# Performance work log

Hardware: AMD Instinct MI355X
Metric: run time of the kernel (lower is better)

## Reference

```python
import jax, jax.numpy as jnp
import numpy as np

THRESH = 0.1
BN_EPS = 1e-5
B, N, C_IN, C_HID, C_OUT = 4096, 128, 64, 256, 128


def setup_inputs() -> dict:
    key = jax.random.key(0)
    ks = jax.random.split(key, 10)
    a = jax.random.uniform(ks[0], (B, N, N), dtype=jnp.float32)
    v = jax.random.normal(ks[1], (B, N, C_IN), dtype=jnp.float32)
    # MLP params: Linear(C_IN->C_HID) + BN + ReLU + Linear(C_HID->C_OUT) + BN + ReLU
    W1 = jax.random.normal(ks[2], (C_IN, C_HID), dtype=jnp.float32) / np.sqrt(C_IN)
    b1 = jnp.zeros((C_HID,), jnp.float32)
    g1 = 1.0 + 0.1 * jax.random.normal(ks[3], (C_HID,), dtype=jnp.float32)
    be1 = 0.1 * jax.random.normal(ks[4], (C_HID,), dtype=jnp.float32)
    rm1 = 0.1 * jax.random.normal(ks[5], (C_HID,), dtype=jnp.float32)
    rv1 = jnp.ones((C_HID,), jnp.float32)
    W2 = jax.random.normal(ks[6], (C_HID, C_OUT), dtype=jnp.float32) / np.sqrt(C_HID)
    b2 = jnp.zeros((C_OUT,), jnp.float32)
    g2 = 1.0 + 0.1 * jax.random.normal(ks[7], (C_OUT,), dtype=jnp.float32)
    be2 = 0.1 * jax.random.normal(ks[8], (C_OUT,), dtype=jnp.float32)
    rm2 = 0.1 * jax.random.normal(ks[9], (C_OUT,), dtype=jnp.float32)
    rv2 = jnp.ones((C_OUT,), jnp.float32)
    return {"a": a, "v": v, "W1": W1, "b1": b1, "g1": g1, "be1": be1, "rm1": rm1, "rv1": rv1,
            "W2": W2, "b2": b2, "g2": g2, "be2": be2, "rm2": rm2, "rv2": rv2}


def reference(a, v, W1, b1, g1, be1, rm1, rv1, W2, b2, g2, be2, rm2, rv2):
    # threshold adjacency
    a_th = (a >= THRESH).astype(v.dtype)            # [B, N, N]
    # D^-0.5 A D^-0.5 as row/col rescaling (equivalent to diag_embed + bmm)
    d_inv_sqrt = jnp.sum(a_th, axis=-1) ** -0.5     # [B, N]
    a_bar = d_inv_sqrt[:, :, None] * a_th * d_inv_sqrt[:, None, :]
    # propagate
    h = jnp.einsum('bnm,bmc->bnc', a_bar, v)        # [B, N, C_IN]
    x = h.reshape(-1, h.shape[-1])                  # [(B N), C_IN]
    # MLP with BatchNorm in eval mode (running stats), dropout is identity in eval
    x = x @ W1 + b1
    x = (x - rm1) * jax.lax.rsqrt(rv1 + BN_EPS) * g1 + be1
    x = jax.nn.relu(x)
    x = x @ W2 + b2
    x = (x - rm2) * jax.lax.rsqrt(rv2 + BN_EPS) * g2 + be2
    x = jax.nn.relu(x)
    return x
```

## Files before the change

kernel.cpp:

```cpp
#include <hip/hip_runtime.h>


#define THRESH 0.1f
#define BN_EPS 1e-5f

typedef __attribute__((ext_vector_type(8))) short bf16x8;
typedef __attribute__((ext_vector_type(4))) float f32x4;

__device__ __forceinline__ unsigned short f2bf(float f) {
    union { float f; unsigned u; } x; x.f = f;
    unsigned r = x.u + 0x7FFFu + ((x.u >> 16) & 1u);
    return (unsigned short)(r >> 16);
}

__device__ __forceinline__ unsigned cvt_pk(float lo, float hi) {
    unsigned r;
    asm("v_cvt_pk_bf16_f32 %0, %1, %2" : "=v"(r) : "v"(lo), "v"(hi));
    return r;
}

__global__ void gcn_prep(const float* __restrict__ W1, const float* __restrict__ b1,
                         const float* __restrict__ g1, const float* __restrict__ be1,
                         const float* __restrict__ rm1, const float* __restrict__ rv1,
                         const float* __restrict__ W2, const float* __restrict__ b2,
                         const float* __restrict__ g2, const float* __restrict__ be2,
                         const float* __restrict__ rm2, const float* __restrict__ rv2,
                         unsigned short* __restrict__ W1s, unsigned short* __restrict__ W2s,
                         float* __restrict__ sh1, float* __restrict__ sh2) {
    int t = blockIdx.x * blockDim.x + threadIdx.x;
    if (t < 256 * 64) {
        int n = t >> 6, kp = t & 63;
        int sp = kp >> 3, lo = kp & 7;
        int s  = sp ^ (n & 7);
        int k2 = s * 8 + lo;
        int r = k2 & 3, aa = (k2 >> 2) & 1, gg = (k2 >> 3) & 3, T = k2 >> 5;
        int k = T * 32 + aa * 16 + gg * 4 + r;
        float sc = g1[n] * rsqrtf(rv1[n] + BN_EPS);
        W1s[t] = f2bf(W1[k * 256 + n] * sc);
    }
    {
        int n = t >> 8, kp = t & 255;
        int sp = kp >> 3, lo = kp & 7;
        int s  = sp ^ (n & 7);
        int k2 = s * 8 + lo;
        int r = k2 & 3, aa = (k2 >> 2) & 1, gg = (k2 >> 3) & 3, T = k2 >> 5;
        int k = T * 32 + aa * 16 + gg * 4 + r;
        float sc = g2[n] * rsqrtf(rv2[n] + BN_EPS);
        W2s[t] = f2bf(W2[k * 128 + n] * sc);
    }
    if (t < 256) {
        float s = g1[t] * rsqrtf(rv1[t] + BN_EPS);
        sh1[t] = (b1[t] - rm1[t]) * s + be1[t];
    }
    if (t < 128) {
        float s = g2[t] * rsqrtf(rv2[t] + BN_EPS);
        sh2[t] = (b2[t] - rm2[t]) * s + be2[t];
    }
}

__global__ void __launch_bounds__(256, 4)
gcn_prop(const float* __restrict__ A, const float* __restrict__ V,
         unsigned short* __restrict__ hP) {
    __shared__ unsigned short s_vtt[64 * 136];

    const int t    = threadIdx.x;
    const int lane = t & 63;
    const int w    = t >> 6;
    const int r16  = lane & 15;
    const int g    = lane >> 4;
    const int b    = blockIdx.x;

    const int mloc  = lane & 31;
    const int chalf = (lane >> 5) * 32;
    const float* vb = V + (size_t)b * 8192 + (size_t)(32 * w + mloc) * 64 + chalf;
    f32x4 pv[8];
#pragma unroll
    for (int q = 0; q < 8; ++q) pv[q] = *(const f32x4*)(vb + 4 * q);

    const float* ab = A + (size_t)b * 16384 + (size_t)(32 * w + r16) * 128;
    bf16x8 afrag[2][4];
    int cnt0 = 0, cnt1 = 0;
#pragma unroll
    for (int mt = 0; mt < 2; ++mt)
#pragma unroll
        for (int ks = 0; ks < 4; ++ks) {
            const float* p = ab + mt * 2048 + ks * 32 + 8 * g;
            f32x4 x0 = *(const f32x4*)p;
            f32x4 x1 = *(const f32x4*)(p + 4);
            union { unsigned short s[8]; bf16x8 v; } u;
            u.s[0] = (x0.x >= THRESH) ? (unsigned short)0x3F80u : (unsigned short)0u;
            u.s[1] = (x0.y >= THRESH) ? (unsigned short)0x3F80u : (unsigned short)0u;
            u.s[2] = (x0.z >= THRESH) ? (unsigned short)0x3F80u : (unsigned short)0u;
            u.s[3] = (x0.w >= THRESH) ? (unsigned short)0x3F80u : (unsigned short)0u;
            u.s[4] = (x1.x >= THRESH) ? (unsigned short)0x3F80u : (unsigned short)0u;
            u.s[5] = (x1.y >= THRESH) ? (unsigned short)0x3F80u : (unsigned short)0u;
            u.s[6] = (x1.z >= THRESH) ? (unsigned short)0x3F80u : (unsigned short)0u;
            u.s[7] = (x1.w >= THRESH) ? (unsigned short)0x3F80u : (unsigned short)0u;
            afrag[mt][ks] = u.v;
            int c = (x0.x >= THRESH) + (x0.y >= THRESH) + (x0.z >= THRESH) + (x0.w >= THRESH)
                  + (x1.x >= THRESH) + (x1.y >= THRESH) + (x1.z >= THRESH) + (x1.w >= THRESH);
            if (mt == 0) cnt0 += c; else cnt1 += c;
        }
    cnt0 += __shfl_xor(cnt0, 16); cnt0 += __shfl_xor(cnt0, 32);
    cnt1 += __shfl_xor(cnt1, 16); cnt1 += __shfl_xor(cnt1, 32);
    const float dinv0 = rsqrtf((float)cnt0);
    const float dinv1 = rsqrtf((float)cnt1);

    {
        float dm = (lane & 16) ? dinv1 : dinv0;
        int m = 32 * w + mloc;
#pragma unroll
        for (int q = 0; q < 8; ++q) {
            int c = chalf + 4 * q;
            s_vtt[(c + 0) * 136 + m] = f2bf(pv[q].x * dm);
            s_vtt[(c + 1) * 136 + m] = f2bf(pv[q].y * dm);
            s_vtt[(c + 2) * 136 + m] = f2bf(pv[q].z * dm);
            s_vtt[(c + 3) * 136 + m] = f2bf(pv[q].w * dm);
        }
    }
    __syncthreads();

    f32x4 acc1[4][2];
#pragma unroll
    for (int ct = 0; ct < 4; ++ct)
#pragma unroll
        for (int mt = 0; mt < 2; ++mt) acc1[ct][mt] = f32x4{0.f, 0.f, 0.f, 0.f};
#pragma unroll
    for (int ks = 0; ks < 4; ++ks)
#pragma unroll
        for (int ct = 0; ct < 4; ++ct) {
            bf16x8 av = *(const bf16x8*)(s_vtt + (ct * 16 + r16) * 136 + ks * 32 + 8 * g);
            acc1[ct][0] = __builtin_amdgcn_mfma_f32_16x16x32_bf16(av, afrag[0][ks], acc1[ct][0], 0, 0, 0);
            acc1[ct][1] = __builtin_amdgcn_mfma_f32_16x16x32_bf16(av, afrag[1][ks], acc1[ct][1], 0, 0, 0);
        }

#pragma unroll
    for (int mt = 0; mt < 2; ++mt) {
        float d = (mt == 0) ? dinv0 : dinv1;
        size_t m = (size_t)(b * 128 + 32 * w + 16 * mt + r16);
#pragma unroll
        for (int ks2 = 0; ks2 < 2; ++ks2) {
            union { unsigned u[4]; bf16x8 v; } pk;
            pk.u[0] = cvt_pk(acc1[2 * ks2][mt][0] * d,     acc1[2 * ks2][mt][1] * d);
            pk.u[1] = cvt_pk(acc1[2 * ks2][mt][2] * d,     acc1[2 * ks2][mt][3] * d);
            pk.u[2] = cvt_pk(acc1[2 * ks2 + 1][mt][0] * d, acc1[2 * ks2 + 1][mt][1] * d);
            pk.u[3] = cvt_pk(acc1[2 * ks2 + 1][mt][2] * d, acc1[2 * ks2 + 1][mt][3] * d);
            *(bf16x8*)(hP + m * 64 + ks2 * 32 + 8 * g) = pk.v;
        }
    }
}

__global__ void __launch_bounds__(512, 2)
gcn_mlp(const unsigned short* __restrict__ hP,
        const unsigned short* __restrict__ W1s, const unsigned short* __restrict__ W2s,
        const float* __restrict__ sh1g, const float* __restrict__ sh2g,
        float* __restrict__ out) {
    __shared__ char smem[99840];
    unsigned short* W1L = (unsigned short*)smem;
    unsigned short* W2L = (unsigned short*)(smem + 32768);
    float* s_sh1 = (float*)(smem + 98304);
    float* s_sh2 = (float*)(smem + 99328);

    const int t    = threadIdx.x;
    const int lane = t & 63;
    const int w    = t >> 6;
    const int r16  = lane & 15;
    const int g    = lane >> 4;

#pragma unroll
    for (int q = 0; q < 4; ++q)
        *(f32x4*)(smem + t * 64 + q * 16) = *(const f32x4*)((const char*)W1s + t * 64 + q * 16);
#pragma unroll
    for (int q = 0; q < 8; ++q)
        *(f32x4*)(smem + 32768 + t * 128 + q * 16) =
            *(const f32x4*)((const char*)W2s + t * 128 + q * 16);
    if (t < 256) s_sh1[t] = sh1g[t];
    if (t < 128) s_sh2[t] = sh2g[t];
    __syncthreads();

    const size_t row00 = (size_t)blockIdx.x * 1024;

#pragma unroll 1
    for (int i = 0; i < 4; ++i) {
        const size_t mb = row00 + (size_t)i * 256 + 32 * w;

        bf16x8 bh[2][2];
#pragma unroll
        for (int mt = 0; mt < 2; ++mt)
#pragma unroll
            for (int ks2 = 0; ks2 < 2; ++ks2)
                bh[mt][ks2] = *(const bf16x8*)(hP + (mb + 16 * mt + r16) * 64 + ks2 * 32 + 8 * g);

        f32x4 acc3[2][8];
#pragma unroll
        for (int mt = 0; mt < 2; ++mt)
#pragma unroll
            for (int ct = 0; ct < 8; ++ct) acc3[mt][ct] = f32x4{0.f, 0.f, 0.f, 0.f};

#pragma unroll
        for (int T = 0; T < 8; ++T) {
            f32x4 a2[2][2];
#pragma unroll
            for (int mt = 0; mt < 2; ++mt)
#pragma unroll
                for (int ctp = 0; ctp < 2; ++ctp) a2[mt][ctp] = f32x4{0.f, 0.f, 0.f, 0.f};
#pragma unroll
            for (int ctp = 0; ctp < 2; ++ctp) {
                int n = (2 * T + ctp) * 16 + r16;
#pragma unroll
                for (int ks2 = 0; ks2 < 2; ++ks2) {
                    int sp = (ks2 * 4 + g) ^ (n & 7);
                    bf16x8 aw = *(const bf16x8*)(W1L + n * 64 + sp * 8);
                    a2[0][ctp] = __builtin_amdgcn_mfma_f32_16x16x32_bf16(aw, bh[0][ks2], a2[0][ctp], 0, 0, 0);
                    a2[1][ctp] = __builtin_amdgcn_mfma_f32_16x16x32_bf16(aw, bh[1][ks2], a2[1][ctp], 0, 0, 0);
                }
            }
            union { unsigned u[4]; bf16x8 v; } af[2];
#pragma unroll
            for (int ctp = 0; ctp < 2; ++ctp) {
                f32x4 sh = *(const f32x4*)(s_sh1 + (2 * T + ctp) * 16 + 4 * g);
#pragma unroll
                for (int mt = 0; mt < 2; ++mt) {
                    float y0 = fmaxf(a2[mt][ctp][0] + sh.x, 0.f);
                    float y1 = fmaxf(a2[mt][ctp][1] + sh.y, 0.f);
                    float y2 = fmaxf(a2[mt][ctp][2] + sh.z, 0.f);
                    float y3 = fmaxf(a2[mt][ctp][3] + sh.w, 0.f);
                    af[mt].u[2 * ctp + 0] = cvt_pk(y0, y1);
                    af[mt].u[2 * ctp + 1] = cvt_pk(y2, y3);
                }
            }
#pragma unroll
            for (int ct3 = 0; ct3 < 8; ++ct3) {
                int n  = ct3 * 16 + r16;
                int sp = (T * 4 + g) ^ (n & 7);
                bf16x8 bw = *(const bf16x8*)(W2L + n * 256 + sp * 8);
                acc3[0][ct3] = __builtin_amdgcn_mfma_f32_16x16x32_bf16(af[0].v, bw, acc3[0][ct3], 0, 0, 0);
                acc3[1][ct3] = __builtin_amdgcn_mfma_f32_16x16x32_bf16(af[1].v, bw, acc3[1][ct3], 0, 0, 0);
            }
        }

        float* ob = out + mb * 128;
#pragma unroll
        for (int ct3 = 0; ct3 < 8; ++ct3) {
            int c = ct3 * 16 + r16;
            float sh = s_sh2[c];
#pragma unroll
            for (int mt = 0; mt < 2; ++mt)
#pragma unroll
                for (int r = 0; r < 4; ++r) {
                    int row = 16 * mt + 4 * g + r;
                    ob[row * 128 + c] = fmaxf(acc3[mt][ct3][r] + sh, 0.f);
                }
        }
    }
}

extern "C" void kernel_launch(void* const* d_in, const int* in_sizes, int n_in,
                              void* d_out, int out_size, void* d_ws, size_t ws_size,
                              hipStream_t stream) {
    (void)in_sizes; (void)n_in; (void)out_size; (void)ws_size;
    const float* a   = (const float*)d_in[0];
    const float* v   = (const float*)d_in[1];
    const float* W1  = (const float*)d_in[2];
    const float* b1  = (const float*)d_in[3];
    const float* g1  = (const float*)d_in[4];
    const float* be1 = (const float*)d_in[5];
    const float* rm1 = (const float*)d_in[6];
    const float* rv1 = (const float*)d_in[7];
    const float* W2  = (const float*)d_in[8];
    const float* b2  = (const float*)d_in[9];
    const float* g2  = (const float*)d_in[10];
    const float* be2 = (const float*)d_in[11];
    const float* rm2 = (const float*)d_in[12];
    const float* rv2 = (const float*)d_in[13];

    char* ws = (char*)d_ws;
    unsigned short* W1s = (unsigned short*)ws;
    unsigned short* W2s = (unsigned short*)(ws + 32768);
    float* sh1 = (float*)(ws + 98304);
    float* sh2 = (float*)(ws + 99328);
    unsigned short* hP = (unsigned short*)(ws + 102400);

    gcn_prep<<<128, 256, 0, stream>>>(W1, b1, g1, be1, rm1, rv1,
                                      W2, b2, g2, be2, rm2, rv2,
                                      W1s, W2s, sh1, sh2);
    gcn_prop<<<4096, 256, 0, stream>>>(a, v, hP);
    gcn_mlp<<<512, 512, 0, stream>>>(hP, W1s, W2s, sh1, sh2, (float*)d_out);
}
```

Measured before the change: 202.7 us.

## Fuse graph propagation and MLP into one persistent kernel

Merges the propagation kernel and the MLP kernel into a single kernel. Each 512-thread block handles 16 graphs, two at a time, and feeds the bf16 propagated features straight from registers into the MLP. This removes the global write and re-read of the intermediate hidden buffer and one kernel launch. In exchange, occupancy drops to one large block per CU and the loads for the next graph happen serially after the output stores, which may expose memory latency.

```diff
diff --git a/kernel.cpp b/kernel.cpp
--- a/kernel.cpp
+++ b/kernel.cpp
@@ -58,114 +58,26 @@
     }
 }
 
-__global__ void __launch_bounds__(256, 4)
-gcn_prop(const float* __restrict__ A, const float* __restrict__ V,
-         unsigned short* __restrict__ hP) {
-    __shared__ unsigned short s_vtt[64 * 136];
+__global__ void __launch_bounds__(512, 1)
+gcn_fused(const float* __restrict__ A, const float* __restrict__ V,
+          const unsigned short* __restrict__ W1s, const unsigned short* __restrict__ W2s,
+          const float* __restrict__ sh1g, const float* __restrict__ sh2g,
+          float* __restrict__ out) {
+    __shared__ char smem[134656];
+    unsigned short* W1L = (unsigned short*)smem;
+    unsigned short* W2L = (unsigned short*)(smem + 32768);
+    float* s_sh1 = (float*)(smem + 133120);
+    float* s_sh2 = (float*)(smem + 134144);
 
     const int t    = threadIdx.x;
     const int lane = t & 63;
     const int w    = t >> 6;
     const int r16  = lane & 15;
     const int g    = lane >> 4;
-    const int b    = blockIdx.x;
-
-    const int mloc  = lane & 31;
-    const int chalf = (lane >> 5) * 32;
-    const float* vb = V + (size_t)b * 8192 + (size_t)(32 * w + mloc) * 64 + chalf;
-    f32x4 pv[8];
-#pragma unroll
-    for (int q = 0; q < 8; ++q) pv[q] = *(const f32x4*)(vb + 4 * q);
-
-    const float* ab = A + (size_t)b * 16384 + (size_t)(32 * w + r16) * 128;
-    bf16x8 afrag[2][4];
-    int cnt0 = 0, cnt1 = 0;
-#pragma unroll
-    for (int mt = 0; mt < 2; ++mt)
-#pragma unroll
-        for (int ks = 0; ks < 4; ++ks) {
-            const float* p = ab + mt * 2048 + ks * 32 + 8 * g;
-            f32x4 x0 = *(const f32x4*)p;
-            f32x4 x1 = *(const f32x4*)(p + 4);
-            union { unsigned short s[8]; bf16x8 v; } u;
-            u.s[0] = (x0.x >= THRESH) ? (unsigned short)0x3F80u : (unsigned short)0u;
-            u.s[1] = (x0.y >= THRESH) ? (unsigned short)0x3F80u : (unsigned short)0u;
-            u.s[2] = (x0.z >= THRESH) ? (unsigned short)0x3F80u : (unsigned short)0u;
-            u.s[3] = (x0.w >= THRESH) ? (unsigned short)0x3F80u : (unsigned short)0u;
-            u.s[4] = (x1.x >= THRESH) ? (unsigned short)0x3F80u : (unsigned short)0u;
-            u.s[5] = (x1.y >= THRESH) ? (unsigned short)0x3F80u : (unsigned short)0u;
-            u.s[6] = (x1.z >= THRESH) ? (unsigned short)0x3F80u : (unsigned short)0u;
-            u.s[7] = (x1.w >= THRESH) ? (unsigned short)0x3F80u : (unsigned short)0u;
-            afrag[mt][ks] = u.v;
-            int c = (x0.x >= THRESH) + (x0.y >= THRESH) + (x0.z >= THRESH) + (x0.w >= THRESH)
-                  + (x1.x >= THRESH) + (x1.y >= THRESH) + (x1.z >= THRESH) + (x1.w >= THRESH);
-            if (mt == 0) cnt0 += c; else cnt1 += c;
-        }
-    cnt0 += __shfl_xor(cnt0, 16); cnt0 += __shfl_xor(cnt0, 32);
-    cnt1 += __shfl_xor(cnt1, 16); cnt1 += __shfl_xor(cnt1, 32);
-    const float dinv0 = rsqrtf((float)cnt0);
-    const float dinv1 = rsqrtf((float)cnt1);
-
-    {
-        float dm = (lane & 16) ? dinv1 : dinv0;
-        int m = 32 * w + mloc;
-#pragma unroll
-        for (int q = 0; q < 8; ++q) {
-            int c = chalf + 4 * q;
-            s_vtt[(c + 0) * 136 + m] = f2bf(pv[q].x * dm);
-            s_vtt[(c + 1) * 136 + m] = f2bf(pv[q].y * dm);
-            s_vtt[(c + 2) * 136 + m] = f2bf(pv[q].z * dm);
-            s_vtt[(c + 3) * 136 + m] = f2bf(pv[q].w * dm);
-        }
-    }
-    __syncthreads();
-
-    f32x4 acc1[4][2];
-#pragma unroll
-    for (int ct = 0; ct < 4; ++ct)
-#pragma unroll
-        for (int mt = 0; mt < 2; ++mt) acc1[ct][mt] = f32x4{0.f, 0.f, 0.f, 0.f};
-#pragma unroll
-    for (int ks = 0; ks < 4; ++ks)
-#pragma unroll
-        for (int ct = 0; ct < 4; ++ct) {
-            bf16x8 av = *(const bf16x8*)(s_vtt + (ct * 16 + r16) * 136 + ks * 32 + 8 * g);
-            acc1[ct][0] = __builtin_amdgcn_mfma_f32_16x16x32_bf16(av, afrag[0][ks], acc1[ct][0], 0, 0, 0);
-            acc1[ct][1] = __builtin_amdgcn_mfma_f32_16x16x32_bf16(av, afrag[1][ks], acc1[ct][1], 0, 0, 0);
-        }
-
-#pragma unroll
-    for (int mt = 0; mt < 2; ++mt) {
-        float d = (mt == 0) ? dinv0 : dinv1;
-        size_t m = (size_t)(b * 128 + 32 * w + 16 * mt + r16);
-#pragma unroll
-        for (int ks2 = 0; ks2 < 2; ++ks2) {
-            union { unsigned u[4]; bf16x8 v; } pk;
-            pk.u[0] = cvt_pk(acc1[2 * ks2][mt][0] * d,     acc1[2 * ks2][mt][1] * d);
-            pk.u[1] = cvt_pk(acc1[2 * ks2][mt][2] * d,     acc1[2 * ks2][mt][3] * d);
-            pk.u[2] = cvt_pk(acc1[2 * ks2 + 1][mt][0] * d, acc1[2 * ks2 + 1][mt][1] * d);
-            pk.u[3] = cvt_pk(acc1[2 * ks2 + 1][mt][2] * d, acc1[2 * ks2 + 1][mt][3] * d);
-            *(bf16x8*)(hP + m * 64 + ks2 * 32 + 8 * g) = pk.v;
-        }
-    }
-}
-
-__global__ void __launch_bounds__(512, 2)
-gcn_mlp(const unsigned short* __restrict__ hP,
-        const unsigned short* __restrict__ W1s, const unsigned short* __restrict__ W2s,
-        const float* __restrict__ sh1g, const float* __restrict__ sh2g,
-        float* __restrict__ out) {
-    __shared__ char smem[99840];
-    unsigned short* W1L = (unsigned short*)smem;
-    unsigned short* W2L = (unsigned short*)(smem + 32768);
-    float* s_sh1 = (float*)(smem + 98304);
-    float* s_sh2 = (float*)(smem + 99328);
-
-    const int t    = threadIdx.x;
-    const int lane = t & 63;
-    const int w    = t >> 6;
-    const int r16  = lane & 15;
-    const int g    = lane >> 4;
+    const int bs   = w >> 2;
+    const int wl   = w & 3;
+
+    unsigned short* vt = (unsigned short*)(smem + 98304) + bs * (64 * 136);
 
 #pragma unroll
     for (int q = 0; q < 4; ++q)
@@ -176,20 +88,95 @@
             *(const f32x4*)((const char*)W2s + t * 128 + q * 16);
     if (t < 256) s_sh1[t] = sh1g[t];
     if (t < 128) s_sh2[t] = sh2g[t];
+
+    const size_t b00 = (size_t)blockIdx.x * 16;
+
+    const int mloc  = lane & 31;
+    const int chalf = (lane >> 5) * 32;
+
+    bf16x8 afrag[2][4];
+    float dinv0, dinv1;
+    {
+        const size_t b = b00 + bs;
+        const float* vb = V + b * 8192 + (size_t)(32 * wl + mloc) * 64 + chalf;
+        f32x4 pv[8];
+#pragma unroll
+        for (int q = 0; q < 8; ++q) pv[q] = *(const f32x4*)(vb + 4 * q);
+
+        const float* ab = A + b * 16384 + (size_t)(32 * wl + r16) * 128;
+        int cnt0 = 0, cnt1 = 0;
+#pragma unroll
+        for (int mt = 0; mt < 2; ++mt)
+#pragma unroll
+            for (int ks = 0; ks < 4; ++ks) {
+                const float* p = ab + mt * 2048 + ks * 32 + 8 * g;
+                f32x4 x0 = *(const f32x4*)p;
+                f32x4 x1 = *(const f32x4*)(p + 4);
+                union { unsigned short s[8]; bf16x8 v; } u;
+                u.s[0] = (x0.x >= THRESH) ? (unsigned short)0x3F80u : (unsigned short)0u;
+                u.s[1] = (x0.y >= THRESH) ? (unsigned short)0x3F80u : (unsigned short)0u;
+                u.s[2] = (x0.z >= THRESH) ? (unsigned short)0x3F80u : (unsigned short)0u;
+                u.s[3] = (x0.w >= THRESH) ? (unsigned short)0x3F80u : (unsigned short)0u;
+                u.s[4] = (x1.x >= THRESH) ? (unsigned short)0x3F80u : (unsigned short)0u;
+                u.s[5] = (x1.y >= THRESH) ? (unsigned short)0x3F80u : (unsigned short)0u;
+                u.s[6] = (x1.z >= THRESH) ? (unsigned short)0x3F80u : (unsigned short)0u;
+                u.s[7] = (x1.w >= THRESH) ? (unsigned short)0x3F80u : (unsigned short)0u;
+                afrag[mt][ks] = u.v;
+                int c = (x0.x >= THRESH) + (x0.y >= THRESH) + (x0.z >= THRESH) + (x0.w >= THRESH)
+                      + (x1.x >= THRESH) + (x1.y >= THRESH) + (x1.z >= THRESH) + (x1.w >= THRESH);
+                if (mt == 0) cnt0 += c; else cnt1 += c;
+            }
+        cnt0 += __shfl_xor(cnt0, 16); cnt0 += __shfl_xor(cnt0, 32);
+        cnt1 += __shfl_xor(cnt1, 16); cnt1 += __shfl_xor(cnt1, 32);
+        dinv0 = rsqrtf((float)cnt0);
+        dinv1 = rsqrtf((float)cnt1);
+
+        float dm = (lane & 16) ? dinv1 : dinv0;
+        int m = 32 * wl + mloc;
+#pragma unroll
+        for (int q = 0; q < 8; ++q) {
+            int c = chalf + 4 * q;
+            vt[(c + 0) * 136 + m] = f2bf(pv[q].x * dm);
+            vt[(c + 1) * 136 + m] = f2bf(pv[q].y * dm);
+            vt[(c + 2) * 136 + m] = f2bf(pv[q].z * dm);
+            vt[(c + 3) * 136 + m] = f2bf(pv[q].w * dm);
+        }
+    }
     __syncthreads();
 
-    const size_t row00 = (size_t)blockIdx.x * 1024;
-
 #pragma unroll 1
-    for (int i = 0; i < 4; ++i) {
-        const size_t mb = row00 + (size_t)i * 256 + 32 * w;
-
+    for (int it = 0; it < 8; ++it) {
+        const size_t b  = b00 + it * 2 + bs;
+        const size_t mb = (size_t)(32 * wl);
+
+        f32x4 acc1[4][2];
+#pragma unroll
+        for (int ct = 0; ct < 4; ++ct)
+#pragma unroll
+            for (int mt = 0; mt < 2; ++mt) acc1[ct][mt] = f32x4{0.f, 0.f, 0.f, 0.f};
+#pragma unroll
+        for (int ks = 0; ks < 4; ++ks)
+#pragma unroll
+            for (int ct = 0; ct < 4; ++ct) {
+                bf16x8 av = *(const bf16x8*)(vt + (ct * 16 + r16) * 136 + ks * 32 + 8 * g);
+                acc1[ct][0] = __builtin_amdgcn_mfma_f32_16x16x32_bf16(av, afrag[0][ks], acc1[ct][0], 0, 0, 0);
+                acc1[ct][1] = __builtin_amdgcn_mfma_f32_16x16x32_bf16(av, afrag[1][ks], acc1[ct][1], 0, 0, 0);
+            }
         bf16x8 bh[2][2];
 #pragma unroll
-        for (int mt = 0; mt < 2; ++mt)
-#pragma unroll
-            for (int ks2 = 0; ks2 < 2; ++ks2)
-                bh[mt][ks2] = *(const bf16x8*)(hP + (mb + 16 * mt + r16) * 64 + ks2 * 32 + 8 * g);
+        for (int mt = 0; mt < 2; ++mt) {
+            float d = (mt == 0) ? dinv0 : dinv1;
+#pragma unroll
+            for (int ks2 = 0; ks2 < 2; ++ks2) {
+                union { unsigned u[4]; bf16x8 v; } pk;
+                pk.u[0] = cvt_pk(acc1[2 * ks2][mt][0] * d,     acc1[2 * ks2][mt][1] * d);
+                pk.u[1] = cvt_pk(acc1[2 * ks2][mt][2] * d,     acc1[2 * ks2][mt][3] * d);
+                pk.u[2] = cvt_pk(acc1[2 * ks2 + 1][mt][0] * d, acc1[2 * ks2 + 1][mt][1] * d);
+                pk.u[3] = cvt_pk(acc1[2 * ks2 + 1][mt][2] * d, acc1[2 * ks2 + 1][mt][3] * d);
+                bh[mt][ks2] = pk.v;
+            }
+        }
+        __syncthreads();
 
         f32x4 acc3[2][8];
 #pragma unroll
@@ -239,7 +226,7 @@
             }
         }
 
-        float* ob = out + mb * 128;
+        float* ob = out + (b * 128 + mb) * 128;
 #pragma unroll
         for (int ct3 = 0; ct3 < 8; ++ct3) {
             int c = ct3 * 16 + r16;
@@ -251,6 +238,54 @@
                     int row = 16 * mt + 4 * g + r;
                     ob[row * 128 + c] = fmaxf(acc3[mt][ct3][r] + sh, 0.f);
                 }
+        }
+
+        if (it < 7) {
+            const size_t bn = b00 + (it + 1) * 2 + bs;
+            const float* vb = V + bn * 8192 + (size_t)(32 * wl + mloc) * 64 + chalf;
+            f32x4 pv[8];
+#pragma unroll
+            for (int q = 0; q < 8; ++q) pv[q] = *(const f32x4*)(vb + 4 * q);
+
+            const float* ab = A + bn * 16384 + (size_t)(32 * wl + r16) * 128;
+            int cnt0 = 0, cnt1 = 0;
+#pragma unroll
+            for (int mt = 0; mt < 2; ++mt)
+#pragma unroll
+                for (int ks = 0; ks < 4; ++ks) {
+                    const float* p = ab + mt * 2048 + ks * 32 + 8 * g;
+                    f32x4 x0 = *(const f32x4*)p;
+                    f32x4 x1 = *(const f32x4*)(p + 4);
+                    union { unsigned short s[8]; bf16x8 v; } u;
+                    u.s[0] = (x0.x >= THRESH) ? (unsigned short)0x3F80u : (unsigned short)0u;
+                    u.s[1] = (x0.y >= THRESH) ? (unsigned short)0x3F80u : (unsigned short)0u;
+                    u.s[2] = (x0.z >= THRESH) ? (unsigned short)0x3F80u : (unsigned short)0u;
+                    u.s[3] = (x0.w >= THRESH) ? (unsigned short)0x3F80u : (unsigned short)0u;
+                    u.s[4] = (x1.x >= THRESH) ? (unsigned short)0x3F80u : (unsigned short)0u;
+                    u.s[5] = (x1.y >= THRESH) ? (unsigned short)0x3F80u : (unsigned short)0u;
+                    u.s[6] = (x1.z >= THRESH) ? (unsigned short)0x3F80u : (unsigned short)0u;
+                    u.s[7] = (x1.w >= THRESH) ? (unsigned short)0x3F80u : (unsigned short)0u;
+                    afrag[mt][ks] = u.v;
+                    int c = (x0.x >= THRESH) + (x0.y >= THRESH) + (x0.z >= THRESH) + (x0.w >= THRESH)
+                          + (x1.x >= THRESH) + (x1.y >= THRESH) + (x1.z >= THRESH) + (x1.w >= THRESH);
+                    if (mt == 0) cnt0 += c; else cnt1 += c;
+                }
+            cnt0 += __shfl_xor(cnt0, 16); cnt0 += __shfl_xor(cnt0, 32);
+            cnt1 += __shfl_xor(cnt1, 16); cnt1 += __shfl_xor(cnt1, 32);
+            dinv0 = rsqrtf((float)cnt0);
+            dinv1 = rsqrtf((float)cnt1);
+
+            float dm = (lane & 16) ? dinv1 : dinv0;
+            int m = 32 * wl + mloc;
+#pragma unroll
+            for (int q = 0; q < 8; ++q) {
+                int c = chalf + 4 * q;
+                vt[(c + 0) * 136 + m] = f2bf(pv[q].x * dm);
+                vt[(c + 1) * 136 + m] = f2bf(pv[q].y * dm);
+                vt[(c + 2) * 136 + m] = f2bf(pv[q].z * dm);
+                vt[(c + 3) * 136 + m] = f2bf(pv[q].w * dm);
+            }
+            __syncthreads();
         }
     }
 }
@@ -279,11 +314,9 @@
     unsigned short* W2s = (unsigned short*)(ws + 32768);
     float* sh1 = (float*)(ws + 98304);
     float* sh2 = (float*)(ws + 99328);
-    unsigned short* hP = (unsigned short*)(ws + 102400);
 
     gcn_prep<<<128, 256, 0, stream>>>(W1, b1, g1, be1, rm1, rv1,
                                       W2, b2, g2, be2, rm2, rv2,
                                       W1s, W2s, sh1, sh2);
-    gcn_prop<<<4096, 256, 0, stream>>>(a, v, hP);
-    gcn_mlp<<<512, 512, 0, stream>>>(hP, W1s, W2s, sh1, sh2, (float*)d_out);
-}
+    gcn_fused<<<256, 512, 0, stream>>>(a, v, W1s, W2s, sh1, sh2, (float*)d_out);
+}
```

New measurement: 189.5 us (median of 2 runs). 6.5% less time.
